# Optimization experiments

Hardware: AMD Instinct MI355X
Metric: run time of the kernel (lower is better)

## Reference

```python
import jax, jax.numpy as jnp
import numpy as np

N_NODES = 100000
NEG_SLOPE = 0.2


def gat_conv(x, edge_src, edge_dst, W, att_src, att_dst, bias):
    """PyG-style GATConv with heads=1. edge_src/edge_dst include self-loops.
    x: [N, F_in], W: [F_in, F_out], att_src/att_dst: [F_out], bias: [F_out].
    """
    n = x.shape[0]
    h = x @ W  # [N, F_out]
    a_src = h @ att_src  # [N]
    a_dst = h @ att_dst  # [N]
    e = jax.nn.leaky_relu(a_src[edge_src] + a_dst[edge_dst], NEG_SLOPE)  # [E]
    # segment softmax over edges sharing a destination node
    m = jax.ops.segment_max(e, edge_dst, num_segments=n)  # [N]; self-loops ensure no empty segment
    p = jnp.exp(e - m[edge_dst])
    denom = jax.ops.segment_sum(p, edge_dst, num_segments=n)  # [N]
    alpha = p / denom[edge_dst]  # [E]
    out = jax.ops.segment_sum(alpha[:, None] * h[edge_src], edge_dst, num_segments=n)
    return out + bias


def setup_inputs() -> dict:
    key = jax.random.key(0)
    ks = jax.random.split(key, 16)
    n, e = N_NODES, 1_600_000
    f_in, f_hid, f_out = 128, 64, 32
    x = jax.random.normal(ks[0], (n, f_in), dtype=jnp.float32)
    edge_index = jax.random.randint(ks[1], (2, e), 0, n, dtype=jnp.int32)

    def lin(k, fi, fo):
        return jax.random.normal(k, (fi, fo), dtype=jnp.float32) / np.sqrt(fi).astype(np.float32)

    def att(k, fo):
        return jax.random.normal(k, (fo,), dtype=jnp.float32) / np.sqrt(fo).astype(np.float32)

    return {
        "x": x, "edge_index": edge_index,
        "W1": lin(ks[2], f_in, f_hid), "as1": att(ks[3], f_hid), "ad1": att(ks[4], f_hid),
        "b1": jnp.zeros((f_hid,), jnp.float32),
        "W2": lin(ks[5], f_hid, f_hid), "as2": att(ks[6], f_hid), "ad2": att(ks[7], f_hid),
        "b2": jnp.zeros((f_hid,), jnp.float32),
        "W3": lin(ks[8], f_hid, f_out), "as3": att(ks[9], f_out), "ad3": att(ks[10], f_out),
        "b3": jnp.zeros((f_out,), jnp.float32),
    }


def reference(x, edge_index, W1, as1, ad1, b1, W2, as2, ad2, b2, W3, as3, ad3, b3):
    n = x.shape[0]
    # PyG GATConv default add_self_loops=True
    loops = jnp.arange(n, dtype=edge_index.dtype)
    src = jnp.concatenate([edge_index[0], loops])
    dst = jnp.concatenate([edge_index[1], loops])

    h1 = jax.nn.relu(gat_conv(x, src, dst, W1, as1, ad1, b1))
    h2 = jax.nn.relu(gat_conv(h1, src, dst, W2, as2, ad2, b2))
    out = gat_conv(h2, src, dst, W3, as3, ad3, b3)
    return (out, h1, h2)
```

## Files before the change

kernel.cpp:

```cpp
#include <hip/hip_runtime.h>
#include <hip/hip_bf16.h>

#define NEG_SLOPE 0.2f

__device__ __forceinline__ unsigned short bf16bits(float f) {
    __hip_bfloat16 t = __float2bfloat16(f);
    return *reinterpret_cast<unsigned short*>(&t);
}

template <int FIN, int FOUT>
__global__ __launch_bounds__(256) void node_linear(
    const float* __restrict__ x, const float* __restrict__ W,
    const float* __restrict__ att_s, const float* __restrict__ att_d,
    __hip_bfloat16* __restrict__ h, float* __restrict__ a_s, float* __restrict__ a_d, int n)
{
    constexpr int FG = FOUT / 4;
    constexpr int NG = 256 / FG;
    constexpr int NB = NG * 4;
    constexpr int RS = FIN + 4;
    __shared__ float xs[NB * RS];

    const int tid = threadIdx.x;
    const int base = blockIdx.x * NB;

    constexpr int CNT = NB * FIN / 4 / 256;
    #pragma unroll
    for (int i = 0; i < CNT; ++i) {
        int f4 = tid + 256 * i;
        int node = f4 / (FIN / 4);
        int kk = f4 % (FIN / 4);
        float4 v = make_float4(0.f, 0.f, 0.f, 0.f);
        if (base + node < n) v = *(const float4*)(x + (size_t)(base + node) * FIN + kk * 4);
        *(float4*)(xs + node * RS + kk * 4) = v;
    }
    __syncthreads();

    const int fg = tid % FG;
    const int ng = tid / FG;
    const float* wp = W + fg * 4;
    const float* xr0 = xs + (ng * 4 + 0) * RS;
    const float* xr1 = xs + (ng * 4 + 1) * RS;
    const float* xr2 = xs + (ng * 4 + 2) * RS;
    const float* xr3 = xs + (ng * 4 + 3) * RS;

    float a00=0,a01=0,a02=0,a03=0, a10=0,a11=0,a12=0,a13=0;
    float a20=0,a21=0,a22=0,a23=0, a30=0,a31=0,a32=0,a33=0;
    #pragma unroll 4
    for (int k = 0; k < FIN; ++k) {
        float4 w = *(const float4*)(wp + (size_t)k * FOUT);
        float x0 = xr0[k], x1 = xr1[k], x2 = xr2[k], x3 = xr3[k];
        a00 = fmaf(x0, w.x, a00); a01 = fmaf(x0, w.y, a01);
        a02 = fmaf(x0, w.z, a02); a03 = fmaf(x0, w.w, a03);
        a10 = fmaf(x1, w.x, a10); a11 = fmaf(x1, w.y, a11);
        a12 = fmaf(x1, w.z, a12); a13 = fmaf(x1, w.w, a13);
        a20 = fmaf(x2, w.x, a20); a21 = fmaf(x2, w.y, a21);
        a22 = fmaf(x2, w.z, a22); a23 = fmaf(x2, w.w, a23);
        a30 = fmaf(x3, w.x, a30); a31 = fmaf(x3, w.y, a31);
        a32 = fmaf(x3, w.z, a32); a33 = fmaf(x3, w.w, a33);
    }

    const float4 ats = *(const float4*)(att_s + fg * 4);
    const float4 atd = *(const float4*)(att_d + fg * 4);
    float acc[4][4] = {{a00,a01,a02,a03},{a10,a11,a12,a13},
                       {a20,a21,a22,a23},{a30,a31,a32,a33}};
    #pragma unroll
    for (int i = 0; i < 4; ++i) {
        int node = base + ng * 4 + i;
        float ps = acc[i][0]*ats.x + acc[i][1]*ats.y + acc[i][2]*ats.z + acc[i][3]*ats.w;
        float pd = acc[i][0]*atd.x + acc[i][1]*atd.y + acc[i][2]*atd.z + acc[i][3]*atd.w;
        #pragma unroll
        for (int o = FG / 2; o > 0; o >>= 1) {
            ps += __shfl_xor(ps, o);
            pd += __shfl_xor(pd, o);
        }
        if (fg == 0 && node < n) { a_s[node] = ps; a_d[node] = pd; }
        if (node < n) {
            unsigned w0 = (unsigned)bf16bits(acc[i][0]) | ((unsigned)bf16bits(acc[i][1]) << 16);
            unsigned w1 = (unsigned)bf16bits(acc[i][2]) | ((unsigned)bf16bits(acc[i][3]) << 16);
            uint2 pk; pk.x = w0; pk.y = w1;
            *reinterpret_cast<uint2*>(h + (size_t)node * FOUT + fg * 4) = pk;
        }
    }
}


__global__ void node_hist(const int* __restrict__ edst, int E, int n,
                          int* __restrict__ cnt)
{
    int i = blockIdx.x * blockDim.x + threadIdx.x;
    const int Etot = E + n;
    if (i >= Etot) return;
    int d = (i < E) ? edst[i] : i - E;
    atomicAdd(cnt + d, 1);
}

__global__ __launch_bounds__(1024) void scan_block(
    const int* __restrict__ cnt, int n, int* __restrict__ row, int* __restrict__ partials)
{
    __shared__ int buf[1024];
    int gid = blockIdx.x * 1024 + threadIdx.x;
    int v = (gid < n) ? cnt[gid] : 0;
    buf[threadIdx.x] = v;
    __syncthreads();
    for (int off = 1; off < 1024; off <<= 1) {
        int t = (threadIdx.x >= off) ? buf[threadIdx.x - off] : 0;
        __syncthreads();
        buf[threadIdx.x] += t;
        __syncthreads();
    }
    if (gid < n) row[gid] = buf[threadIdx.x] - v;
    if (threadIdx.x == 1023) partials[blockIdx.x] = buf[1023];
}

__global__ __launch_bounds__(128) void scan_partials(int* __restrict__ partials, int nb)
{
    __shared__ int buf[128];
    int v = (threadIdx.x < nb) ? partials[threadIdx.x] : 0;
    buf[threadIdx.x] = v;
    __syncthreads();
    for (int off = 1; off < 128; off <<= 1) {
        int t = (threadIdx.x >= off) ? buf[threadIdx.x - off] : 0;
        __syncthreads();
        buf[threadIdx.x] += t;
        __syncthreads();
    }
    if (threadIdx.x < nb) partials[threadIdx.x] = buf[threadIdx.x] - v;
}

__global__ __launch_bounds__(1024) void scan_add(
    int* __restrict__ row, int n, const int* __restrict__ partials,
    const int* __restrict__ cnt, int* __restrict__ row_end)
{
    int gid = blockIdx.x * 1024 + threadIdx.x;
    if (gid < n) {
        int r = row[gid] + partials[blockIdx.x];
        row[gid] = r;
        row_end[gid] = r + cnt[gid];
    }
}

__global__ void init_sbcur(const int* __restrict__ row, int n, int nsb,
                           int* __restrict__ sbcur)
{
    int i = blockIdx.x * blockDim.x + threadIdx.x;
    if (i < nsb) sbcur[i] = row[i << 9];
}

#define CB_CHUNK 4096
#define CB_NSB_MAX 256
__global__ __launch_bounds__(256) void chunk_bin(
    const int* __restrict__ esrc, const int* __restrict__ edst, int E, int n,
    int nsb, int* __restrict__ sbcur, int* __restrict__ packed1)
{
    __shared__ int pk[CB_CHUNK];
    __shared__ unsigned short sbv[CB_CHUNK];
    __shared__ int hist[CB_NSB_MAX];
    __shared__ int gbase[CB_NSB_MAX];
    const int tid = threadIdx.x;
    const int i0 = blockIdx.x * CB_CHUNK;
    const int Etot = E + n;

    hist[tid] = 0;
    __syncthreads();

    for (int j = tid; j < CB_CHUNK; j += 256) {
        int i = i0 + j;
        if (i < Etot) {
            int s, d;
            if (i < E) { s = esrc[i]; d = edst[i]; }
            else       { s = d = i - E; }
            int sb = d >> 9;
            pk[j] = ((d & 511) << 17) | s;
            sbv[j] = (unsigned short)sb;
            atomicAdd(&hist[sb], 1);
        } else {
            sbv[j] = 0xFFFFu;
        }
    }
    __syncthreads();

    if (tid < nsb && hist[tid] > 0)
        gbase[tid] = atomicAdd(&sbcur[tid], hist[tid]);
    hist[tid] = 0;
    __syncthreads();

    for (int j = tid; j < CB_CHUNK; j += 256) {
        unsigned short sb = sbv[j];
        if (sb != 0xFFFFu) {
            int pos = gbase[sb] + atomicAdd(&hist[sb], 1);
            packed1[pos] = pk[j];
        }
    }
}

__global__ __launch_bounds__(256) void sb_sort(
    const int* __restrict__ row, const int* __restrict__ packed1,
    int* __restrict__ col, int n, int Etot)
{
    const int sb = blockIdx.x;
    const int node0 = sb << 9;
    __shared__ int cur[512];
    for (int i = threadIdx.x; i < 512; i += 256) {
        int node = node0 + i;
        cur[i] = (node < n) ? row[node] : 0;
    }
    __syncthreads();
    const int lo = row[node0];
    const int nxt = node0 + 512;
    const int hi = (nxt < n) ? row[nxt] : Etot;
    for (int j = lo + threadIdx.x; j < hi; j += 256) {
        int p = packed1[j];
        int ld = ((unsigned)p) >> 17;
        int pos = atomicAdd(&cur[ld], 1);
        col[pos] = p & 0x1FFFF;
    }
}

template <int FOUT>
__global__ __launch_bounds__(256) void gat_aggregate(
    const int* __restrict__ row_end, const int* __restrict__ col,
    const float* __restrict__ a_s, const float* __restrict__ a_d,
    const __hip_bfloat16* __restrict__ h, const float* __restrict__ bias,
    float* __restrict__ outp, int n, int do_relu)
{
    constexpr int NPW = 64 / FOUT;
    const int gwave = (blockIdx.x * 256 + threadIdx.x) >> 6;
    const int lane = threadIdx.x & 63;
    const int node = gwave * NPW + lane / FOUT;
    const int f = lane % FOUT;
    if (node >= n) return;
    const int end = row_end[node];
    const int start = (node == 0) ? 0 : row_end[node - 1];
    const float adn = a_d[node];
    const int egrp = (FOUT == 64) ? 0 : (lane & 32);
    float acc = 0.f, den = 0.f;
    for (int j = start; j < end; j += 8) {
        int k_idx = j + (lane & 7);
        int clamped = (k_idx < end) ? k_idx : (end - 1);
        int sown = col[clamped];
        float eown = a_s[sown] + adn;
        eown = (eown > 0.f) ? eown : NEG_SLOPE * eown;
        float pown = (k_idx < end) ? __expf(eown) : 0.f;
        #pragma unroll
        for (int k = 0; k < 8; ++k) {
            int  sk = __shfl(sown, egrp + k);
            float pk = __shfl(pown, egrp + k);
            den += pk;
            acc = fmaf(pk, __bfloat162float(h[(size_t)sk * FOUT + f]), acc);
        }
    }
    float v = acc / den + bias[f];
    if (do_relu) v = fmaxf(v, 0.f);
    outp[(size_t)node * FOUT + f] = v;
}

extern "C" void kernel_launch(void* const* d_in, const int* in_sizes, int n_in,
                              void* d_out, int out_size, void* d_ws, size_t ws_size,
                              hipStream_t stream)
{
    const float* x   = (const float*)d_in[0];
    const int* eidx  = (const int*)d_in[1];
    const float* W1  = (const float*)d_in[2];
    const float* as1 = (const float*)d_in[3];
    const float* ad1 = (const float*)d_in[4];
    const float* b1  = (const float*)d_in[5];
    const float* W2  = (const float*)d_in[6];
    const float* as2 = (const float*)d_in[7];
    const float* ad2 = (const float*)d_in[8];
    const float* b2  = (const float*)d_in[9];
    const float* W3  = (const float*)d_in[10];
    const float* as3 = (const float*)d_in[11];
    const float* ad3 = (const float*)d_in[12];
    const float* b3  = (const float*)d_in[13];

    const int fhid = in_sizes[3];
    const int fin  = in_sizes[2] / fhid;
    const int fo3  = in_sizes[11];
    const int n    = in_sizes[0] / fin;
    const int E    = in_sizes[1] / 2;
    const int Etot = E + n;
    const int nsb  = (n + 511) >> 9;

    const int* esrc = eidx;
    const int* edst = eidx + E;

    float* out = (float*)d_out;
    float* h1  = out + (size_t)n * fo3;
    float* h2  = h1 + (size_t)n * fhid;

    int* cnt      = (int*)d_ws;
    int* row      = cnt + n;
    int* row_end  = row + n;
    int* partials = row_end + n;
    int* sbcur    = partials + 128;
    int* packed1  = sbcur + 256;
    int* col      = packed1 + Etot;
    __hip_bfloat16* h = (__hip_bfloat16*)(col + Etot);
    float* a_s    = (float*)(h + (size_t)n * fhid);
    float* a_d    = a_s + n;

    const int EB = (Etot + 255) / 256;
    const int nb = (n + 1023) / 1024;
    const int nchunks = (Etot + CB_CHUNK - 1) / CB_CHUNK;

    hipMemsetAsync(cnt, 0, (size_t)n * 4, stream);
    node_hist<<<EB, 256, 0, stream>>>(edst, E, n, cnt);
    scan_block<<<nb, 1024, 0, stream>>>(cnt, n, row, partials);
    scan_partials<<<1, 128, 0, stream>>>(partials, nb);
    scan_add<<<nb, 1024, 0, stream>>>(row, n, partials, cnt, row_end);
    init_sbcur<<<(nsb + 255) / 256, 256, 0, stream>>>(row, n, nsb, sbcur);
    chunk_bin<<<nchunks, 256, 0, stream>>>(esrc, edst, E, n, nsb, sbcur, packed1);
    sb_sort<<<nsb, 256, 0, stream>>>(row, packed1, col, n, Etot);

    const int NLB64  = (n + 63) / 64;
    const int NLB128 = (n + 127) / 128;
    const int AGG64 = (n + 3) / 4;
    const int AGG32 = (n + 7) / 8;

    node_linear<128, 64><<<NLB64, 256, 0, stream>>>(x, W1, as1, ad1, h, a_s, a_d, n);
    gat_aggregate<64><<<AGG64, 256, 0, stream>>>(row_end, col, a_s, a_d, h, b1, h1, n, 1);

    node_linear<64, 64><<<NLB64, 256, 0, stream>>>(h1, W2, as2, ad2, h, a_s, a_d, n);
    gat_aggregate<64><<<AGG64, 256, 0, stream>>>(row_end, col, a_s, a_d, h, b2, h2, n, 1);

    node_linear<64, 32><<<NLB128, 256, 0, stream>>>(h2, W3, as3, ad3, h, a_s, a_d, n);
    gat_aggregate<32><<<AGG32, 256, 0, stream>>>(row_end, col, a_s, a_d, h, b3, out, n, 0);
}
```

Measured before the change: 353.2 us.

## Build CSR via superblock histogram and per-block local scan instead of global node scan

Replaces the per-node global histogram plus three-kernel scan with a 512-node superblock histogram (shared-memory atomics) and a single-block scan. Each superblock then counts its nodes' degrees and does a local scan in sb_sort2 to produce row_end and scatter positions. This removes the 1.7M global atomics into the per-node count array, the memset of n ints, and several small launches, in exchange for an extra pass over packed1 inside each sort block.

```diff
diff --git a/kernel.cpp b/kernel.cpp
--- a/kernel.cpp
+++ b/kernel.cpp
@@ -84,66 +84,44 @@
 }
 
 
-__global__ void node_hist(const int* __restrict__ edst, int E, int n,
-                          int* __restrict__ cnt)
-{
-    int i = blockIdx.x * blockDim.x + threadIdx.x;
+__global__ __launch_bounds__(256) void sb_hist(
+    const int* __restrict__ edst, int E, int n, int* __restrict__ sbhist)
+{
+    __shared__ int lh[256];
+    const int tid = threadIdx.x;
+    lh[tid] = 0;
+    __syncthreads();
     const int Etot = E + n;
-    if (i >= Etot) return;
-    int d = (i < E) ? edst[i] : i - E;
-    atomicAdd(cnt + d, 1);
-}
-
-__global__ __launch_bounds__(1024) void scan_block(
-    const int* __restrict__ cnt, int n, int* __restrict__ row, int* __restrict__ partials)
-{
-    __shared__ int buf[1024];
-    int gid = blockIdx.x * 1024 + threadIdx.x;
-    int v = (gid < n) ? cnt[gid] : 0;
-    buf[threadIdx.x] = v;
-    __syncthreads();
-    for (int off = 1; off < 1024; off <<= 1) {
-        int t = (threadIdx.x >= off) ? buf[threadIdx.x - off] : 0;
+    const int stride = gridDim.x * 256;
+    for (int i = blockIdx.x * 256 + tid; i < Etot; i += stride) {
+        int d = (i < E) ? edst[i] : i - E;
+        atomicAdd(&lh[d >> 9], 1);
+    }
+    __syncthreads();
+    if (lh[tid] > 0) atomicAdd(&sbhist[tid], lh[tid]);
+}
+
+__global__ __launch_bounds__(256) void sb_scan(
+    const int* __restrict__ sbhist, int nsb, int Etot,
+    int* __restrict__ sbbase, int* __restrict__ sbcur)
+{
+    __shared__ int buf[256];
+    const int tid = threadIdx.x;
+    int v = (tid < nsb) ? sbhist[tid] : 0;
+    buf[tid] = v;
+    __syncthreads();
+    for (int off = 1; off < 256; off <<= 1) {
+        int t = (tid >= off) ? buf[tid - off] : 0;
         __syncthreads();
-        buf[threadIdx.x] += t;
+        buf[tid] += t;
         __syncthreads();
     }
-    if (gid < n) row[gid] = buf[threadIdx.x] - v;
-    if (threadIdx.x == 1023) partials[blockIdx.x] = buf[1023];
-}
-
-__global__ __launch_bounds__(128) void scan_partials(int* __restrict__ partials, int nb)
-{
-    __shared__ int buf[128];
-    int v = (threadIdx.x < nb) ? partials[threadIdx.x] : 0;
-    buf[threadIdx.x] = v;
-    __syncthreads();
-    for (int off = 1; off < 128; off <<= 1) {
-        int t = (threadIdx.x >= off) ? buf[threadIdx.x - off] : 0;
-        __syncthreads();
-        buf[threadIdx.x] += t;
-        __syncthreads();
-    }
-    if (threadIdx.x < nb) partials[threadIdx.x] = buf[threadIdx.x] - v;
-}
-
-__global__ __launch_bounds__(1024) void scan_add(
-    int* __restrict__ row, int n, const int* __restrict__ partials,
-    const int* __restrict__ cnt, int* __restrict__ row_end)
-{
-    int gid = blockIdx.x * 1024 + threadIdx.x;
-    if (gid < n) {
-        int r = row[gid] + partials[blockIdx.x];
-        row[gid] = r;
-        row_end[gid] = r + cnt[gid];
-    }
-}
-
-__global__ void init_sbcur(const int* __restrict__ row, int n, int nsb,
-                           int* __restrict__ sbcur)
-{
-    int i = blockIdx.x * blockDim.x + threadIdx.x;
-    if (i < nsb) sbcur[i] = row[i << 9];
+    if (tid < nsb) {
+        int ex = buf[tid] - v;
+        sbbase[tid] = ex;
+        sbcur[tid] = ex;
+    }
+    if (tid == 0) sbbase[nsb] = Etot;
 }
 
 #define CB_CHUNK 4096
@@ -193,25 +171,44 @@
     }
 }
 
-__global__ __launch_bounds__(256) void sb_sort(
-    const int* __restrict__ row, const int* __restrict__ packed1,
-    int* __restrict__ col, int n, int Etot)
+__global__ __launch_bounds__(256) void sb_sort2(
+    const int* __restrict__ sbbase, const int* __restrict__ packed1,
+    int* __restrict__ col, int* __restrict__ row_end, int n)
 {
     const int sb = blockIdx.x;
     const int node0 = sb << 9;
-    __shared__ int cur[512];
-    for (int i = threadIdx.x; i < 512; i += 256) {
+    const int lo = sbbase[sb];
+    const int hi = sbbase[sb + 1];
+    const int tid = threadIdx.x;
+    __shared__ int c[512];
+    __shared__ int sc[512];
+    c[tid] = 0; c[tid + 256] = 0;
+    __syncthreads();
+    for (int j = lo + tid; j < hi; j += 256)
+        atomicAdd(&c[((unsigned)packed1[j]) >> 17], 1);
+    __syncthreads();
+    sc[tid] = c[tid]; sc[tid + 256] = c[tid + 256];
+    __syncthreads();
+    for (int off = 1; off < 512; off <<= 1) {
+        int i0 = tid, i1 = tid + 256;
+        int v0 = (i0 >= off) ? sc[i0 - off] : 0;
+        int v1 = (i1 >= off) ? sc[i1 - off] : 0;
+        __syncthreads();
+        sc[i0] += v0; sc[i1] += v1;
+        __syncthreads();
+    }
+    #pragma unroll
+    for (int q = 0; q < 2; ++q) {
+        int i = tid + q * 256;
         int node = node0 + i;
-        cur[i] = (node < n) ? row[node] : 0;
-    }
-    __syncthreads();
-    const int lo = row[node0];
-    const int nxt = node0 + 512;
-    const int hi = (nxt < n) ? row[nxt] : Etot;
-    for (int j = lo + threadIdx.x; j < hi; j += 256) {
+        if (node < n) row_end[node] = lo + sc[i];
+        c[i] = lo + sc[i] - c[i];
+    }
+    __syncthreads();
+    for (int j = lo + tid; j < hi; j += 256) {
         int p = packed1[j];
         int ld = ((unsigned)p) >> 17;
-        int pos = atomicAdd(&cur[ld], 1);
+        int pos = atomicAdd(&c[ld], 1);
         col[pos] = p & 0x1FFFF;
     }
 }
@@ -288,29 +285,23 @@
     float* h1  = out + (size_t)n * fo3;
     float* h2  = h1 + (size_t)n * fhid;
 
-    int* cnt      = (int*)d_ws;
-    int* row      = cnt + n;
-    int* row_end  = row + n;
-    int* partials = row_end + n;
-    int* sbcur    = partials + 128;
-    int* packed1  = sbcur + 256;
+    int* sbhist   = (int*)d_ws;
+    int* sbbase   = sbhist + 256;
+    int* sbcur    = sbbase + 260;
+    int* row_end  = sbcur + 256;
+    int* packed1  = row_end + n;
     int* col      = packed1 + Etot;
     __hip_bfloat16* h = (__hip_bfloat16*)(col + Etot);
     float* a_s    = (float*)(h + (size_t)n * fhid);
     float* a_d    = a_s + n;
 
-    const int EB = (Etot + 255) / 256;
-    const int nb = (n + 1023) / 1024;
     const int nchunks = (Etot + CB_CHUNK - 1) / CB_CHUNK;
 
-    hipMemsetAsync(cnt, 0, (size_t)n * 4, stream);
-    node_hist<<<EB, 256, 0, stream>>>(edst, E, n, cnt);
-    scan_block<<<nb, 1024, 0, stream>>>(cnt, n, row, partials);
-    scan_partials<<<1, 128, 0, stream>>>(partials, nb);
-    scan_add<<<nb, 1024, 0, stream>>>(row, n, partials, cnt, row_end);
-    init_sbcur<<<(nsb + 255) / 256, 256, 0, stream>>>(row, n, nsb, sbcur);
+    hipMemsetAsync(sbhist, 0, 256 * 4, stream);
+    sb_hist<<<1024, 256, 0, stream>>>(edst, E, n, sbhist);
+    sb_scan<<<1, 256, 0, stream>>>(sbhist, nsb, Etot, sbbase, sbcur);
     chunk_bin<<<nchunks, 256, 0, stream>>>(esrc, edst, E, n, nsb, sbcur, packed1);
-    sb_sort<<<nsb, 256, 0, stream>>>(row, packed1, col, n, Etot);
+    sb_sort2<<<nsb, 256, 0, stream>>>(sbbase, packed1, col, row_end, n);
 
     const int NLB64  = (n + 63) / 64;
     const int NLB128 = (n + 127) / 128;
```

New measurement: 323.9 us. -8.3%, faster.
